# Performance work log

Measured on AMD Instinct MI355X. Metric: run time of the kernel, lower is better.

Reference implementation:

```python
import jax, jax.numpy as jnp
import numpy as np

B, L, D = 2, 4096, 1024
H, HD = 16, D // 16
W = 256          # window_size
C = 256          # chunk/block size (== W, so each block sees prev + current block)
NC = L // C
SCALE = HD ** -0.5


def complex_linear(z, Wr, Wi):
    # z: [..., D, 2]; W*: [out, in] (torch Linear convention y = x @ W^T)
    xr, xi = z[..., 0], z[..., 1]
    yr = jnp.einsum('...i,oi->...o', xr, Wr) - jnp.einsum('...i,oi->...o', xi, Wi)
    yi = jnp.einsum('...i,oi->...o', xr, Wi) + jnp.einsum('...i,oi->...o', xi, Wr)
    return jnp.stack([yr, yi], axis=-1)


def _heads(x):
    # [B, L, D, 2] -> [B, H, NC, C, HD, 2]
    return x.reshape(B, L, H, HD, 2).transpose(0, 2, 1, 3, 4).reshape(B, H, NC, C, HD, 2)


def _band_mask():
    # block c, query local qi (global i = c*C + qi), key local kj over [prev block | cur block]
    # global j = (c-1)*C + kj ; valid iff 0 <= j <= i and i - j < W
    c = jnp.arange(NC)[:, None, None]
    qi = jnp.arange(C)[None, :, None]
    kj = jnp.arange(2 * C)[None, None, :]
    i = c * C + qi
    j = (c - 1) * C + kj
    return (j >= 0) & (j <= i) & (i - j < W)  # [NC, C, 2C]


def setup_inputs() -> dict:
    key = jax.random.key(0)
    ks = jax.random.split(key, 9)
    s = D ** -0.5
    inp = {'z': jax.random.normal(ks[0], (B, L, D, 2), jnp.float32)}
    names = ['Wq_r', 'Wq_i', 'Wk_r', 'Wk_i', 'Wv_r', 'Wv_i', 'Wo_r', 'Wo_i']
    for n, k in zip(names, ks[1:]):
        inp[n] = jax.random.normal(k, (D, D), jnp.float32) * s
    return inp


def reference(z, Wq_r, Wq_i, Wk_r, Wk_i, Wv_r, Wv_i, Wo_r, Wo_i):
    q = _heads(complex_linear(z, Wq_r, Wq_i))  # [B,H,NC,C,HD,2]
    k = _heads(complex_linear(z, Wk_r, Wk_i))
    v = _heads(complex_linear(z, Wv_r, Wv_i))

    def with_prev(x):  # [B,H,NC,C,HD,2] -> [B,H,NC,2C,HD,2] (prev block | cur block)
        prev = jnp.concatenate([jnp.zeros_like(x[:, :, :1]), x[:, :, :-1]], axis=2)
        return jnp.concatenate([prev, x], axis=3)

    kc = with_prev(k)
    vc = with_prev(v)

    # Re(q * conj(k)) = qr*kr + qi*ki
    scores = (jnp.einsum('bhncd,bhnkd->bhnck', q[..., 0], kc[..., 0])
              + jnp.einsum('bhncd,bhnkd->bhnck', q[..., 1], kc[..., 1])) * SCALE
    scores = jnp.where(_band_mask()[None, None], scores, -jnp.inf)
    w = jax.nn.softmax(scores, axis=-1)  # [B,H,NC,C,2C]

    out_r = jnp.einsum('bhnck,bhnkd->bhncd', w, vc[..., 0])
    out_i = jnp.einsum('bhnck,bhnkd->bhncd', w, vc[..., 1])
    out = jnp.stack([out_r, out_i], axis=-1)           # [B,H,NC,C,HD,2]
    out = out.reshape(B, H, L, HD, 2).transpose(0, 2, 1, 3, 4).reshape(B, L, D, 2)
    return complex_linear(out, Wo_r, Wo_i)
```

## Files before the change

kernel.cpp:

```cpp
#include <hip/hip_runtime.h>
#include <hip/hip_bf16.h>
#include <stdint.h>


typedef __attribute__((ext_vector_type(8))) short bf16x8;
typedef __attribute__((ext_vector_type(8))) unsigned short u16x8;
typedef __attribute__((ext_vector_type(4))) float f32x4;

#define PA_SCALE 0.125f
#define UNR _Pragma("unroll")

__device__ __forceinline__ unsigned short f2bf(float f) {
  unsigned int u = __builtin_bit_cast(unsigned int, f);
  u += 0x7fffu + ((u >> 16) & 1u);
  return (unsigned short)(u >> 16);
}

#define GLD16(gp, lp)                                          \
  __builtin_amdgcn_global_load_lds(                            \
      (const __attribute__((address_space(1))) void*)(gp),     \
      (__attribute__((address_space(3))) void*)(lp), 16, 0, 0)

__global__ __launch_bounds__(256) void pa_pack_A(const float* __restrict__ z,
                                                 unsigned short* __restrict__ A1) {
  int idx = (blockIdx.x * 256 + threadIdx.x) * 8;
  int m = idx >> 10, d = idx & 1023;
  const float2* zp = (const float2*)z + idx;
  u16x8 re, im;
  UNR for (int j = 0; j < 8; ++j) {
    float2 f = zp[j];
    re[j] = f2bf(f.x);
    im[j] = f2bf(f.y);
  }
  *(u16x8*)(A1 + (size_t)m * 2048 + d)        = re;
  *(u16x8*)(A1 + (size_t)m * 2048 + 1024 + d) = im;
}

__global__ __launch_bounds__(256) void pa_pack_B(
    const float* __restrict__ Wq_r, const float* __restrict__ Wq_i,
    const float* __restrict__ Wk_r, const float* __restrict__ Wk_i,
    const float* __restrict__ Wv_r, const float* __restrict__ Wv_i,
    const float* __restrict__ Wo_r, const float* __restrict__ Wo_i,
    unsigned short* __restrict__ Bp) {
  int idx = (blockIdx.x * 256 + threadIdx.x) * 8;
  int n = idx >> 10, d = idx & 1023;
  int proj = n >> 11, part = (n >> 10) & 1, o = n & 1023;
  const float* Wr; const float* Wi;
  if (proj == 0)      { Wr = Wq_r; Wi = Wq_i; }
  else if (proj == 1) { Wr = Wk_r; Wi = Wk_i; }
  else if (proj == 2) { Wr = Wv_r; Wi = Wv_i; }
  else                { Wr = Wo_r; Wi = Wo_i; }
  const float* pr = Wr + (size_t)o * 1024 + d;
  const float* pi = Wi + (size_t)o * 1024 + d;
  u16x8 lo, hi;
  UNR for (int j = 0; j < 8; ++j) {
    float r = pr[j], im = pi[j];
    if (part == 0) { lo[j] = f2bf(r);  hi[j] = f2bf(-im); }
    else           { lo[j] = f2bf(im); hi[j] = f2bf(r);  }
  }
  size_t nn = (proj < 3) ? (size_t)n : (size_t)(6144 + o * 2 + part);
  *(u16x8*)(Bp + nn * 2048 + d)        = lo;
  *(u16x8*)(Bp + nn * 2048 + 1024 + d) = hi;
}

#define BARR()                              \
  do {                                      \
    __builtin_amdgcn_s_barrier();           \
    __builtin_amdgcn_sched_barrier(0);      \
  } while (0)

#define READ_A(P, MH)                                                         \
  UNR for (int i = 0; i < 4; ++i)                                             \
    UNR for (int ks = 0; ks < 2; ++ks)                                        \
      af[i][ks] = *(const bf16x8*)&lds[P][MH][aoff + i * 1024 +               \
                                              ((ks * 32 + koff) ^ cxor)];

#define READ_B(P, NH, DST)                                                    \
  UNR for (int j = 0; j < 2; ++j)                                             \
    UNR for (int ks = 0; ks < 2; ++ks)                                        \
      DST[j][ks] = *(const bf16x8*)&lds[P][2 + (NH)][boff + j * 1024 +        \
                                                     ((ks * 32 + koff) ^ cxor)];

#define MFMA_Q(MB, NB, BF)                                                    \
  UNR for (int ks = 0; ks < 2; ++ks)                                          \
    UNR for (int i = 0; i < 4; ++i)                                           \
      UNR for (int j = 0; j < 2; ++j)                                         \
        acc[(MB) + i][(NB) + j] = __builtin_amdgcn_mfma_f32_16x16x32_bf16(    \
            af[i][ks], BF[j][ks], acc[(MB) + i][(NB) + j], 0, 0, 0);

#define TILE(P, T)                                                            \
  {                                                                           \
    READ_A(P, 0);                                                             \
    READ_B(P, 0, b0);                                                         \
    stageB(0, (T) + 1);                                                       \
    BARR();                                                                   \
    __builtin_amdgcn_s_setprio(1);                                            \
    MFMA_Q(0, 0, b0);                                                         \
    __builtin_amdgcn_s_setprio(0);                                            \
    BARR();                                                                   \
    READ_B(P, 1, b1);                                                         \
    stageA(0, (T) + 2);                                                       \
    BARR();                                                                   \
    __builtin_amdgcn_s_setprio(1);                                            \
    MFMA_Q(0, 2, b1);                                                         \
    __builtin_amdgcn_s_setprio(0);                                            \
    BARR();                                                                   \
    READ_A(P, 1);                                                             \
    stageB(1, (T) + 2);                                                       \
    BARR();                                                                   \
    __builtin_amdgcn_s_setprio(1);                                            \
    MFMA_Q(4, 2, b1);                                                         \
    __builtin_amdgcn_s_setprio(0);                                            \
    BARR();                                                                   \
    stageA(1, (T) + 2);                                                       \
    BARR();                                                                   \
    __builtin_amdgcn_s_setprio(1);                                            \
    MFMA_Q(4, 0, b0);                                                         \
    __builtin_amdgcn_s_setprio(0);                                            \
    asm volatile("s_waitcnt vmcnt(6)" ::: "memory");                          \
    __builtin_amdgcn_sched_barrier(0);                                        \
    BARR();                                                                   \
  }

template <int EPI>
__global__ __launch_bounds__(512, 2) void pa_gemm8(
    const unsigned short* __restrict__ A,
    const unsigned short* __restrict__ B,
    void* __restrict__ Cout, int K, int N) {
  __shared__ unsigned short lds[2][4][128 * 64];

  const int tid = threadIdx.x;
  const int lane = tid & 63, wid = tid >> 6;
  const int wm = wid >> 2, wn = wid & 3;
  const int lr = lane & 15, lh = lane >> 4;

  const int nwg = gridDim.x * gridDim.y;
  const int wg = blockIdx.y * gridDim.x + blockIdx.x;
  const int cpx = nwg >> 3;
  const int swz = (wg & 7) * cpx + (wg >> 3);
  const int bx = swz % gridDim.x, by = swz / gridDim.x;
  const int tm0 = by * 256, tn0 = bx * 256;

  const int NT = K >> 6;

  const int srow = lane >> 3;
  const int scolS = ((lane & 7) ^ srow) * 8;

  auto stageA = [&](int half, int ts) {
    int t = ts < NT ? ts : ts - NT;
    const unsigned short* g0 = A + (size_t)(tm0 + half * 128) * K + t * 64 + scolS;
    unsigned short* l0 = &lds[ts & 1][half][0];
    UNR for (int c = 0; c < 2; ++c) {
      int chunk = wid * 2 + c;
      GLD16(g0 + (size_t)(chunk * 8 + srow) * K, l0 + chunk * 512);
    }
  };
  auto stageB = [&](int half, int ts) {
    int t = ts < NT ? ts : ts - NT;
    const unsigned short* g0 = B + (size_t)(tn0 + half * 128) * K + t * 64 + scolS;
    unsigned short* l0 = &lds[ts & 1][2 + half][0];
    UNR for (int c = 0; c < 2; ++c) {
      int chunk = wid * 2 + c;
      GLD16(g0 + (size_t)(chunk * 8 + srow) * K, l0 + chunk * 512);
    }
  };

  const int aoff = (wm * 64 + lr) * 64;
  const int boff = (wn * 32 + lr) * 64;
  const int koff = lh * 8;
  const int cxor = (lr & 7) * 8;

  f32x4 acc[8][4];
  f32x4 zero4 = {0.f, 0.f, 0.f, 0.f};
  UNR for (int i = 0; i < 8; ++i)
    UNR for (int j = 0; j < 4; ++j) acc[i][j] = zero4;

  bf16x8 af[4][2], b0[2][2], b1[2][2];

  stageA(0, 0); stageB(0, 0); stageB(1, 0); stageA(1, 0);
  stageA(0, 1); stageB(1, 1); stageA(1, 1);
  asm volatile("s_waitcnt vmcnt(6)" ::: "memory");
  __builtin_amdgcn_sched_barrier(0);
  __builtin_amdgcn_s_barrier();
  __builtin_amdgcn_sched_barrier(0);

  for (int t = 0; t < NT; t += 2) {
    TILE(0, t);
    TILE(1, t + 1);
  }

  UNR for (int mh = 0; mh < 2; ++mh)
    UNR for (int i = 0; i < 4; ++i)
      UNR for (int nh = 0; nh < 2; ++nh)
        UNR for (int j = 0; j < 2; ++j)
          UNR for (int r = 0; r < 4; ++r) {
            int row = tm0 + mh * 128 + wm * 64 + i * 16 + lh * 4 + r;
            int col = tn0 + nh * 128 + wn * 32 + j * 16 + lr;
            float v = acc[mh * 4 + i][nh * 2 + j][r];
            if (EPI == 0) {
              ((unsigned short*)Cout)[(size_t)row * N + col] = f2bf(v);
            } else {
              ((float*)Cout)[(size_t)row * N + col] = v;
            }
          }
}

#define QK1(SI)                                                               \
  __builtin_amdgcn_s_setprio(1);                                              \
  UNR for (int kk = 0; kk < 2; ++kk)                                          \
    UNR for (int f = 0; f < 4; ++f) {                                         \
      bf16x8 br = *(const bf16x8*)&Ks[0][f * 16 + lr][kk * 32 + lh * 8];      \
      bf16x8 bi = *(const bf16x8*)&Ks[1][f * 16 + lr][kk * 32 + lh * 8];      \
      sac[SI][f] = __builtin_amdgcn_mfma_f32_16x16x32_bf16(qfr[kk], br,       \
                                                           sac[SI][f], 0, 0, 0); \
      sac[SI][f] = __builtin_amdgcn_mfma_f32_16x16x32_bf16(qfi[kk], bi,       \
                                                           sac[SI][f], 0, 0, 0); \
    }                                                                         \
  __builtin_amdgcn_s_setprio(0);

#define PW1(SI)                                                               \
  UNR for (int f = 0; f < 4; ++f)                                             \
    UNR for (int r = 0; r < 4; ++r)                                           \
      Ps[wv][lh * 4 + r][f * 16 + lr] = f2bf(sac[SI][f][r]);

#define PV1()                                                                 \
  {                                                                           \
    bf16x8 pa0 = *(const bf16x8*)&Ps[wv][lr][lh * 8];                         \
    bf16x8 pa1 = *(const bf16x8*)&Ps[wv][lr][32 + lh * 8];                    \
    __builtin_amdgcn_s_setprio(1);                                            \
    UNR for (int kk = 0; kk < 2; ++kk) {                                      \
      bf16x8 pak = kk ? pa1 : pa0;                                            \
      UNR for (int fc = 0; fc < 4; ++fc) {                                    \
        bf16x8 vr = *(const bf16x8*)&Vts[0][fc * 16 + lr][kk * 32 + lh * 8];  \
        bf16x8 vi = *(const bf16x8*)&Vts[1][fc * 16 + lr][kk * 32 + lh * 8];  \
        oac[0][fc] = __builtin_amdgcn_mfma_f32_16x16x32_bf16(pak, vr,         \
                                                             oac[0][fc], 0, 0, 0); \
        oac[1][fc] = __builtin_amdgcn_mfma_f32_16x16x32_bf16(pak, vi,         \
                                                             oac[1][fc], 0, 0, 0); \
      }                                                                       \
    }                                                                         \
    __builtin_amdgcn_s_setprio(0);                                            \
  }

__global__ __launch_bounds__(512) void pa_attn(const unsigned short* __restrict__ C1,
                                               unsigned short* __restrict__ A2) {
  __shared__ unsigned short Ks[2][64][72];
  __shared__ unsigned short Vts[2][64][72];
  __shared__ unsigned short Ps[8][16][72];

  int bid = blockIdx.x;
  int half = bid & 1, nc = (bid >> 1) & 15, h = (bid >> 5) & 15, b = bid >> 9;
  int tid = threadIdx.x;
  int l = tid & 63, wv = tid >> 6;
  int lr = l & 15, lh = l >> 4;
  int base = wv >> 2;

  const int C1LD = 6144;
  const int rowB = b * 4096;
  const int colQr = h * 64,        colQi = 1024 + h * 64;
  const int colKr = 2048 + h * 64, colKi = 3072 + h * 64;
  const int colVr = 4096 + h * 64, colVi = 5120 + h * 64;
  const int q0 = half * 128;
  const int qw = q0 + wv * 16;

  bf16x8 qfr[2], qfi[2];
  {
    const unsigned short* pr = C1 + (size_t)(rowB + nc * 256 + qw + lr) * C1LD + colQr;
    const unsigned short* pi = C1 + (size_t)(rowB + nc * 256 + qw + lr) * C1LD + colQi;
    qfr[0] = *(const bf16x8*)(pr + lh * 8);
    qfr[1] = *(const bf16x8*)(pr + 32 + lh * 8);
    qfi[0] = *(const bf16x8*)(pi + lh * 8);
    qfi[1] = *(const bf16x8*)(pi + 32 + lh * 8);
  }

  f32x4 zero4 = {0.f, 0.f, 0.f, 0.f};
  f32x4 sac[5][4];
#pragma unroll
  for (int c = 0; c < 5; ++c)
#pragma unroll
    for (int f = 0; f < 4; ++f) sac[c][f] = zero4;

#pragma unroll
  for (int c = 0; c < 6; ++c) {
    __syncthreads();
#pragma unroll
    for (int s = 0; s < 2; ++s) {
      int seg = s * 512 + tid;
      int arr = seg >> 9, row = (seg >> 3) & 63, sg = seg & 7;
      int kj = q0 + c * 64 + row;
      int tok = (nc - 1) * 256 + kj; if (tok < 0) tok = 0;
      const unsigned short* src =
          C1 + (size_t)(rowB + tok) * C1LD + (arr ? colKi : colKr) + sg * 8;
      *(bf16x8*)&Ks[arr][row][sg * 8] = *(const bf16x8*)src;
    }
    __syncthreads();
    if (wv < 4) { if (c < 5) { QK1(c); } }
    else        { if (c >= 1) { QK1(c - 1); } }
  }

  float mx[4] = {-1e30f, -1e30f, -1e30f, -1e30f};
#pragma unroll
  for (int si = 0; si < 5; ++si)
#pragma unroll
    for (int f = 0; f < 4; ++f)
#pragma unroll
      for (int r = 0; r < 4; ++r) {
        int qi_ = qw + lh * 4 + r;
        int kj  = q0 + (si + base) * 64 + f * 16 + lr;
        bool valid = (kj > qi_) && (kj <= qi_ + 256) && (nc > 0 || kj >= 256);
        float s = valid ? sac[si][f][r] * PA_SCALE : -1e30f;
        sac[si][f][r] = s;
        mx[r] = fmaxf(mx[r], s);
      }
#pragma unroll
  for (int r = 0; r < 4; ++r)
#pragma unroll
    for (int d = 1; d < 16; d <<= 1) mx[r] = fmaxf(mx[r], __shfl_xor(mx[r], d));

  float sm[4] = {0.f, 0.f, 0.f, 0.f};
#pragma unroll
  for (int si = 0; si < 5; ++si)
#pragma unroll
    for (int f = 0; f < 4; ++f)
#pragma unroll
      for (int r = 0; r < 4; ++r) {
        float p = __expf(sac[si][f][r] - mx[r]);
        sac[si][f][r] = p;
        sm[r] += p;
      }
#pragma unroll
  for (int r = 0; r < 4; ++r)
#pragma unroll
    for (int d = 1; d < 16; d <<= 1) sm[r] += __shfl_xor(sm[r], d);
  float inv[4];
#pragma unroll
  for (int r = 0; r < 4; ++r) inv[r] = 1.0f / sm[r];

  f32x4 oac[2][4];
#pragma unroll
  for (int p = 0; p < 2; ++p)
#pragma unroll
    for (int f = 0; f < 4; ++f) oac[p][f] = zero4;

#pragma unroll
  for (int c = 0; c < 6; ++c) {
    __syncthreads();
#pragma unroll
    for (int s = 0; s < 2; ++s) {
      int seg = s * 512 + tid;
      int arr = seg >> 9, row = (seg >> 3) & 63, sg = seg & 7;
      int kj = q0 + c * 64 + row;
      int tok = (nc - 1) * 256 + kj; if (tok < 0) tok = 0;
      const unsigned short* src =
          C1 + (size_t)(rowB + tok) * C1LD + (arr ? colVi : colVr) + sg * 8;
      bf16x8 v = *(const bf16x8*)src;
#pragma unroll
      for (int j = 0; j < 8; ++j) Vts[arr][sg * 8 + j][row] = (unsigned short)v[j];
    }
    if (wv < 4) { if (c < 5) { PW1(c); } }
    else        { if (c >= 1) { PW1(c - 1); } }
    __syncthreads();
    if (wv < 4) { if (c < 5) { PV1(); } }
    else        { if (c >= 1) { PV1(); } }
  }

#pragma unroll
  for (int fc = 0; fc < 4; ++fc)
#pragma unroll
    for (int r = 0; r < 4; ++r) {
      int m  = rowB + nc * 256 + qw + lh * 4 + r;
      int hd = fc * 16 + lr;
      A2[(size_t)m * 2048 + h * 64 + hd]        = f2bf(oac[0][fc][r] * inv[r]);
      A2[(size_t)m * 2048 + 1024 + h * 64 + hd] = f2bf(oac[1][fc][r] * inv[r]);
    }
}

extern "C" void kernel_launch(void* const* d_in, const int* in_sizes, int n_in,
                              void* d_out, int out_size, void* d_ws, size_t ws_size,
                              hipStream_t stream) {
  const float* z = (const float*)d_in[0];
  unsigned short* A1 = (unsigned short*)d_ws;
  unsigned short* Bp = (unsigned short*)((char*)d_ws + 33554432ull);
  unsigned short* C1 = (unsigned short*)((char*)d_ws + 67108864ull);
  float* out = (float*)d_out;

  pa_pack_A<<<4096, 256, 0, stream>>>(z, A1);
  pa_pack_B<<<4096, 256, 0, stream>>>(
      (const float*)d_in[1], (const float*)d_in[2],
      (const float*)d_in[3], (const float*)d_in[4],
      (const float*)d_in[5], (const float*)d_in[6],
      (const float*)d_in[7], (const float*)d_in[8], Bp);
  pa_gemm8<0><<<dim3(24, 32), 512, 0, stream>>>(A1, Bp, C1, 2048, 6144);
  pa_attn<<<1024, 512, 0, stream>>>(C1, A1);
  pa_gemm8<1><<<dim3(8, 32), 512, 0, stream>>>(A1, Bp + (size_t)6144 * 2048, out,
                                               2048, 2048);
}
```

Before: 381.2 us.

## Double-buffer K/V staging in attention and merge pack kernels

```diff
diff --git a/kernel.cpp b/kernel.cpp
--- a/kernel.cpp
+++ b/kernel.cpp
@@ -21,46 +21,47 @@
       (const __attribute__((address_space(1))) void*)(gp),     \
       (__attribute__((address_space(3))) void*)(lp), 16, 0, 0)
 
-__global__ __launch_bounds__(256) void pa_pack_A(const float* __restrict__ z,
-                                                 unsigned short* __restrict__ A1) {
-  int idx = (blockIdx.x * 256 + threadIdx.x) * 8;
-  int m = idx >> 10, d = idx & 1023;
-  const float2* zp = (const float2*)z + idx;
-  u16x8 re, im;
-  UNR for (int j = 0; j < 8; ++j) {
-    float2 f = zp[j];
-    re[j] = f2bf(f.x);
-    im[j] = f2bf(f.y);
-  }
-  *(u16x8*)(A1 + (size_t)m * 2048 + d)        = re;
-  *(u16x8*)(A1 + (size_t)m * 2048 + 1024 + d) = im;
-}
-
-__global__ __launch_bounds__(256) void pa_pack_B(
+__global__ __launch_bounds__(256) void pa_pack(
+    const float* __restrict__ z,
     const float* __restrict__ Wq_r, const float* __restrict__ Wq_i,
     const float* __restrict__ Wk_r, const float* __restrict__ Wk_i,
     const float* __restrict__ Wv_r, const float* __restrict__ Wv_i,
     const float* __restrict__ Wo_r, const float* __restrict__ Wo_i,
-    unsigned short* __restrict__ Bp) {
-  int idx = (blockIdx.x * 256 + threadIdx.x) * 8;
-  int n = idx >> 10, d = idx & 1023;
-  int proj = n >> 11, part = (n >> 10) & 1, o = n & 1023;
-  const float* Wr; const float* Wi;
-  if (proj == 0)      { Wr = Wq_r; Wi = Wq_i; }
-  else if (proj == 1) { Wr = Wk_r; Wi = Wk_i; }
-  else if (proj == 2) { Wr = Wv_r; Wi = Wv_i; }
-  else                { Wr = Wo_r; Wi = Wo_i; }
-  const float* pr = Wr + (size_t)o * 1024 + d;
-  const float* pi = Wi + (size_t)o * 1024 + d;
-  u16x8 lo, hi;
-  UNR for (int j = 0; j < 8; ++j) {
-    float r = pr[j], im = pi[j];
-    if (part == 0) { lo[j] = f2bf(r);  hi[j] = f2bf(-im); }
-    else           { lo[j] = f2bf(im); hi[j] = f2bf(r);  }
-  }
-  size_t nn = (proj < 3) ? (size_t)n : (size_t)(6144 + o * 2 + part);
-  *(u16x8*)(Bp + nn * 2048 + d)        = lo;
-  *(u16x8*)(Bp + nn * 2048 + 1024 + d) = hi;
+    unsigned short* __restrict__ A1, unsigned short* __restrict__ Bp) {
+  int bid = blockIdx.x, tid = threadIdx.x;
+  if (bid < 4096) {
+    int idx = (bid * 256 + tid) * 8;
+    int m = idx >> 10, d = idx & 1023;
+    const float2* zp = (const float2*)z + idx;
+    u16x8 re, im;
+    UNR for (int j = 0; j < 8; ++j) {
+      float2 f = zp[j];
+      re[j] = f2bf(f.x);
+      im[j] = f2bf(f.y);
+    }
+    *(u16x8*)(A1 + (size_t)m * 2048 + d)        = re;
+    *(u16x8*)(A1 + (size_t)m * 2048 + 1024 + d) = im;
+  } else {
+    int idx = ((bid - 4096) * 256 + tid) * 8;
+    int n = idx >> 10, d = idx & 1023;
+    int proj = n >> 11, part = (n >> 10) & 1, o = n & 1023;
+    const float* Wr; const float* Wi;
+    if (proj == 0)      { Wr = Wq_r; Wi = Wq_i; }
+    else if (proj == 1) { Wr = Wk_r; Wi = Wk_i; }
+    else if (proj == 2) { Wr = Wv_r; Wi = Wv_i; }
+    else                { Wr = Wo_r; Wi = Wo_i; }
+    const float* pr = Wr + (size_t)o * 1024 + d;
+    const float* pi = Wi + (size_t)o * 1024 + d;
+    u16x8 lo, hi;
+    UNR for (int j = 0; j < 8; ++j) {
+      float r = pr[j], im = pi[j];
+      if (part == 0) { lo[j] = f2bf(r);  hi[j] = f2bf(-im); }
+      else           { lo[j] = f2bf(im); hi[j] = f2bf(r);  }
+    }
+    size_t nn = (proj < 3) ? (size_t)n : (size_t)(6144 + o * 2 + part);
+    *(u16x8*)(Bp + nn * 2048 + d)        = lo;
+    *(u16x8*)(Bp + nn * 2048 + 1024 + d) = hi;
+  }
 }
 
 #define BARR()                              \
@@ -205,12 +206,36 @@
           }
 }
 
-#define QK1(SI)                                                               \
+#define STAGEK(C, PB)                                                         \
+  UNR for (int s = 0; s < 2; ++s) {                                           \
+    int seg = s * 512 + tid;                                                  \
+    int arr = seg >> 9, row = (seg >> 3) & 63, sg = seg & 7;                  \
+    int kj = q0 + (C) * 64 + row;                                             \
+    int tok = (nc - 1) * 256 + kj; if (tok < 0) tok = 0;                      \
+    const unsigned short* src =                                               \
+        C1 + (size_t)(rowB + tok) * C1LD + (arr ? colKi : colKr) + sg * 8;    \
+    *(bf16x8*)&pool[PB][arr][row][sg * 8] = *(const bf16x8*)src;              \
+  }
+
+#define STAGEV(C, PB)                                                         \
+  UNR for (int s = 0; s < 2; ++s) {                                           \
+    int seg = s * 512 + tid;                                                  \
+    int arr = seg >> 9, row = (seg >> 3) & 63, sg = seg & 7;                  \
+    int kj = q0 + (C) * 64 + row;                                             \
+    int tok = (nc - 1) * 256 + kj; if (tok < 0) tok = 0;                      \
+    const unsigned short* src =                                               \
+        C1 + (size_t)(rowB + tok) * C1LD + (arr ? colVi : colVr) + sg * 8;    \
+    bf16x8 v = *(const bf16x8*)src;                                           \
+    UNR for (int j = 0; j < 8; ++j)                                           \
+      pool[PB][arr][sg * 8 + j][row] = (unsigned short)v[j];                  \
+  }
+
+#define QK1(SI, PB)                                                           \
   __builtin_amdgcn_s_setprio(1);                                              \
   UNR for (int kk = 0; kk < 2; ++kk)                                          \
     UNR for (int f = 0; f < 4; ++f) {                                         \
-      bf16x8 br = *(const bf16x8*)&Ks[0][f * 16 + lr][kk * 32 + lh * 8];      \
-      bf16x8 bi = *(const bf16x8*)&Ks[1][f * 16 + lr][kk * 32 + lh * 8];      \
+      bf16x8 br = *(const bf16x8*)&pool[PB][0][f * 16 + lr][kk * 32 + lh * 8];\
+      bf16x8 bi = *(const bf16x8*)&pool[PB][1][f * 16 + lr][kk * 32 + lh * 8];\
       sac[SI][f] = __builtin_amdgcn_mfma_f32_16x16x32_bf16(qfr[kk], br,       \
                                                            sac[SI][f], 0, 0, 0); \
       sac[SI][f] = __builtin_amdgcn_mfma_f32_16x16x32_bf16(qfi[kk], bi,       \
@@ -223,7 +248,7 @@
     UNR for (int r = 0; r < 4; ++r)                                           \
       Ps[wv][lh * 4 + r][f * 16 + lr] = f2bf(sac[SI][f][r]);
 
-#define PV1()                                                                 \
+#define PV1(PB)                                                               \
   {                                                                           \
     bf16x8 pa0 = *(const bf16x8*)&Ps[wv][lr][lh * 8];                         \
     bf16x8 pa1 = *(const bf16x8*)&Ps[wv][lr][32 + lh * 8];                    \
@@ -231,8 +256,8 @@
     UNR for (int kk = 0; kk < 2; ++kk) {                                      \
       bf16x8 pak = kk ? pa1 : pa0;                                            \
       UNR for (int fc = 0; fc < 4; ++fc) {                                    \
-        bf16x8 vr = *(const bf16x8*)&Vts[0][fc * 16 + lr][kk * 32 + lh * 8];  \
-        bf16x8 vi = *(const bf16x8*)&Vts[1][fc * 16 + lr][kk * 32 + lh * 8];  \
+        bf16x8 vr = *(const bf16x8*)&pool[PB][0][fc * 16 + lr][kk * 32 + lh * 8]; \
+        bf16x8 vi = *(const bf16x8*)&pool[PB][1][fc * 16 + lr][kk * 32 + lh * 8]; \
         oac[0][fc] = __builtin_amdgcn_mfma_f32_16x16x32_bf16(pak, vr,         \
                                                              oac[0][fc], 0, 0, 0); \
         oac[1][fc] = __builtin_amdgcn_mfma_f32_16x16x32_bf16(pak, vi,         \
@@ -244,8 +269,7 @@
 
 __global__ __launch_bounds__(512) void pa_attn(const unsigned short* __restrict__ C1,
                                                unsigned short* __restrict__ A2) {
-  __shared__ unsigned short Ks[2][64][72];
-  __shared__ unsigned short Vts[2][64][72];
+  __shared__ unsigned short pool[2][2][64][72];
   __shared__ unsigned short Ps[8][16][72];
 
   int bid = blockIdx.x;
@@ -280,22 +304,14 @@
 #pragma unroll
     for (int f = 0; f < 4; ++f) sac[c][f] = zero4;
 
+  STAGEK(0, 0);
+  __syncthreads();
 #pragma unroll
   for (int c = 0; c < 6; ++c) {
+    if (c < 5) { STAGEK(c + 1, (c + 1) & 1); }
+    if (wv < 4) { if (c < 5) { QK1(c, c & 1); } }
+    else        { if (c >= 1) { QK1(c - 1, c & 1); } }
     __syncthreads();
-#pragma unroll
-    for (int s = 0; s < 2; ++s) {
-      int seg = s * 512 + tid;
-      int arr = seg >> 9, row = (seg >> 3) & 63, sg = seg & 7;
-      int kj = q0 + c * 64 + row;
-      int tok = (nc - 1) * 256 + kj; if (tok < 0) tok = 0;
-      const unsigned short* src =
-          C1 + (size_t)(rowB + tok) * C1LD + (arr ? colKi : colKr) + sg * 8;
-      *(bf16x8*)&Ks[arr][row][sg * 8] = *(const bf16x8*)src;
-    }
-    __syncthreads();
-    if (wv < 4) { if (c < 5) { QK1(c); } }
-    else        { if (c >= 1) { QK1(c - 1); } }
   }
 
   float mx[4] = {-1e30f, -1e30f, -1e30f, -1e30f};
@@ -342,26 +358,14 @@
 #pragma unroll
     for (int f = 0; f < 4; ++f) oac[p][f] = zero4;
 
+  STAGEV(0, 0);
+  __syncthreads();
 #pragma unroll
   for (int c = 0; c < 6; ++c) {
+    if (c < 5) { STAGEV(c + 1, (c + 1) & 1); }
+    if (wv < 4) { if (c < 5) { PW1(c); PV1(c & 1); } }
+    else        { if (c >= 1) { PW1(c - 1); PV1(c & 1); } }
     __syncthreads();
-#pragma unroll
-    for (int s = 0; s < 2; ++s) {
-      int seg = s * 512 + tid;
-      int arr = seg >> 9, row = (seg >> 3) & 63, sg = seg & 7;
-      int kj = q0 + c * 64 + row;
-      int tok = (nc - 1) * 256 + kj; if (tok < 0) tok = 0;
-      const unsigned short* src =
-          C1 + (size_t)(rowB + tok) * C1LD + (arr ? colVi : colVr) + sg * 8;
-      bf16x8 v = *(const bf16x8*)src;
-#pragma unroll
-      for (int j = 0; j < 8; ++j) Vts[arr][sg * 8 + j][row] = (unsigned short)v[j];
-    }
-    if (wv < 4) { if (c < 5) { PW1(c); } }
-    else        { if (c >= 1) { PW1(c - 1); } }
-    __syncthreads();
-    if (wv < 4) { if (c < 5) { PV1(); } }
-    else        { if (c >= 1) { PV1(); } }
   }
 
 #pragma unroll
@@ -384,12 +388,12 @@
   unsigned short* C1 = (unsigned short*)((char*)d_ws + 67108864ull);
   float* out = (float*)d_out;
 
-  pa_pack_A<<<4096, 256, 0, stream>>>(z, A1);
-  pa_pack_B<<<4096, 256, 0, stream>>>(
+  pa_pack<<<8192, 256, 0, stream>>>(
+      z,
       (const float*)d_in[1], (const float*)d_in[2],
       (const float*)d_in[3], (const float*)d_in[4],
       (const float*)d_in[5], (const float*)d_in[6],
-      (const float*)d_in[7], (const float*)d_in[8], Bp);
+      (const float*)d_in[7], (const float*)d_in[8], A1, Bp);
   pa_gemm8<0><<<dim3(24, 32), 512, 0, stream>>>(A1, Bp, C1, 2048, 6144);
   pa_attn<<<1024, 512, 0, stream>>>(C1, A1);
   pa_gemm8<1><<<dim3(8, 32), 512, 0, stream>>>(A1, Bp + (size_t)6144 * 2048, out,
```

After: 379.2 us. No clear change (-0.5%).
